# Kernel optimization log

Measured on AMD Instinct MI355X. Metric: run time of the kernel, lower is better.

Reference implementation:

```python
import jax, jax.numpy as jnp
import numpy as np


def _pdists(X):
    # Pairwise Euclidean distances (torch.cdist, p=2) via the Gram trick.
    sq = jnp.sum(X * X, axis=1)                      # (bs,)
    d2 = sq[:, None] + sq[None, :] - 2.0 * (X @ X.T)  # (bs, bs)
    d2 = jnp.maximum(d2, 0.0)
    # safe sqrt: exact forward, finite gradient at 0
    pos = d2 > 0
    return jnp.where(pos, jnp.sqrt(jnp.where(pos, d2, 1.0)), 0.0)


def setup_inputs() -> dict:
    key = jax.random.key(0)
    k1, k2, k3 = jax.random.split(key, 3)
    bs, d = 4096, 512
    n_classes, n_domains = 4, 3
    X = jax.random.normal(k1, (bs, d), dtype=jnp.float32)
    ds = jax.random.randint(k2, (bs,), 0, n_domains, dtype=jnp.int64 if jax.config.read('jax_enable_x64') else jnp.int32)
    y = jax.random.randint(k3, (bs,), 0, n_classes, dtype=jnp.int64 if jax.config.read('jax_enable_x64') else jnp.int32)
    return {"X": X, "ds": ds, "y": y, "n_classes": n_classes, "n_domains": n_domains}


def reference(X, ds, y, n_classes, n_domains):
    # Equivalent to JointCCSA.LSA / JointCCSA.LS with norm=True, assuming every
    # class and domain value appears in the batch (what torch.unique would find).
    dists = _pdists(X)                                # (bs, bs)

    d_lt = ds[:, None] < ds[None, :]                  # domain pair (d1 < d2) ordering
    same_y = y[:, None] == y[None, :]
    y_lt = y[:, None] < y[None, :]                    # class pair (c1 < c2) ordering

    # SA loss: 0.5 * sum over (i,j) with y_i==y_j, ds_i<ds_j
    sa_loss = 0.5 * jnp.sum(jnp.where(same_y & d_lt, dists, 0.0))
    n_sa = n_classes * (n_domains * (n_domains - 1) // 2)
    sa_loss = sa_loss / n_sa

    # S loss: hinge on margin=1, 0.5 * sum over (i,j) with y_i<y_j, ds_i<ds_j
    margin = 1.0
    h = jnp.maximum(0.0, margin - dists)
    s_loss = 0.5 * jnp.sum(jnp.where(y_lt & d_lt, h, 0.0))
    n_s = (n_classes * (n_classes - 1) // 2) * (n_domains * (n_domains - 1) // 2)
    s_loss = s_loss / n_s

    return sa_loss, s_loss
```

## Files before the change

### kernel.cpp

```cpp
#include <hip/hip_runtime.h>
#include <hip/hip_bf16.h>
#include <stdint.h>

#define NROW 4096
#define DIM  512
#define BM   128
#define BN   128
#define BK   32
#define NKT  (DIM / BK)

typedef __attribute__((ext_vector_type(8))) short  short8;
typedef __attribute__((ext_vector_type(4))) float  floatx4;

typedef const __attribute__((address_space(1))) void gvoid_t;
typedef __attribute__((address_space(3))) void       svoid_t;

__device__ __forceinline__ unsigned short f32_to_bf16_rne(float f) {
    unsigned u = __float_as_uint(f);
    u += 0x7FFFu + ((u >> 16) & 1u);
    return (unsigned short)(u >> 16);
}

__global__ __launch_bounds__(256) void prep_kernel(
    const float* __restrict__ X, const int* __restrict__ ds,
    const int* __restrict__ y, unsigned short* __restrict__ Xpre,
    float2* __restrict__ meta, float* __restrict__ out)
{
    const int wave = threadIdx.x >> 6;
    const int lane = threadIdx.x & 63;
    const int row  = blockIdx.x * 4 + wave;
    const float4* xr = (const float4*)(X + (size_t)row * DIM);
    float4 v0 = xr[2 * lane];
    float4 v1 = xr[2 * lane + 1];
    float s = v0.x*v0.x + v0.y*v0.y + v0.z*v0.z + v0.w*v0.w
            + v1.x*v1.x + v1.y*v1.y + v1.z*v1.z + v1.w*v1.w;
    uint4 pk;
    pk.x = f32_to_bf16_rne(v0.x) | ((unsigned)f32_to_bf16_rne(v0.y) << 16);
    pk.y = f32_to_bf16_rne(v0.z) | ((unsigned)f32_to_bf16_rne(v0.w) << 16);
    pk.z = f32_to_bf16_rne(v1.x) | ((unsigned)f32_to_bf16_rne(v1.y) << 16);
    pk.w = f32_to_bf16_rne(v1.z) | ((unsigned)f32_to_bf16_rne(v1.w) << 16);
    const int G     = row >> 3;
    const int l3r   = row & 7;
    const int kt32  = lane >> 2;
    const int chunk = lane & 3;
    const int p     = chunk ^ (row & 3);
    *(uint4*)(Xpre + ((size_t)kt32 * 512 + G) * 256 + l3r * 32 + p * 8) = pk;
    #pragma unroll
    for (int off = 32; off; off >>= 1) s += __shfl_xor(s, off);
    if (lane == 0)
        meta[row] = make_float2(s, __int_as_float(y[row] * 4 + ds[row]));
    if (blockIdx.x == 0 && threadIdx.x < 2) out[threadIdx.x] = 0.0f;
}

__global__ __launch_bounds__(512, 6) void ccsa_kernel(
    const unsigned short* __restrict__ Xpre, const float2* __restrict__ meta,
    const int* __restrict__ ncls, const int* __restrict__ ndom,
    float* __restrict__ out)
{
    __shared__ __align__(16) unsigned short As[2 * BM * BK];
    __shared__ __align__(16) unsigned short Bs[2 * BN * BK];
    __shared__ float red[16];

    const int t = blockIdx.x;
    int r = (int)((sqrtf(8.0f * (float)t + 1.0f) - 1.0f) * 0.5f);
    while ((r + 1) * (r + 2) / 2 <= t) ++r;
    while (r * (r + 1) / 2 > t) --r;
    const int bj_t = r;
    const int bi_t = t - r * (r + 1) / 2;
    const bool diag = (bi_t == bj_t);
    const int bm0 = bi_t * BM;
    const int bn0 = bj_t * BN;
    const int GA = bm0 >> 3;
    const int GB = bn0 >> 3;

    const int tid    = threadIdx.x;
    const int wave   = tid >> 6;
    const int lane   = tid & 63;
    const int warp_m = wave >> 2;
    const int warp_n = wave & 3;
    const int m15    = lane & 15;
    const int quad   = lane >> 4;
    const int sw     = m15 & 3;

    float sqj[2]; int yj[2], dj[2];
    #pragma unroll
    for (int tn = 0; tn < 2; ++tn) {
        const float2 mj = meta[bn0 + warp_n * 32 + tn * 16 + m15];
        sqj[tn] = mj.x;
        const int ydj = __float_as_int(mj.y);
        dj[tn] = ydj & 3; yj[tn] = ydj >> 2;
    }

    floatx4 acc[4][2];
    #pragma unroll
    for (int a = 0; a < 4; ++a)
        #pragma unroll
        for (int b = 0; b < 2; ++b)
            acc[a][b] = (floatx4){0.f, 0.f, 0.f, 0.f};

    const unsigned short* Bbase = diag ? As : Bs;

    #define STAGE(buf, kt)                                                    \
        do {                                                                  \
            __builtin_amdgcn_global_load_lds(                                 \
                (gvoid_t*)(Xpre + ((size_t)(kt) * 512 + GA) * 256 + tid * 8), \
                (svoid_t*)(&As[(buf) * 4096 + tid * 8]), 16, 0, 0);           \
            if (!diag)                                                        \
                __builtin_amdgcn_global_load_lds(                             \
                    (gvoid_t*)(Xpre + ((size_t)(kt) * 512 + GB) * 256         \
                               + tid * 8),                                    \
                    (svoid_t*)(&Bs[(buf) * 4096 + tid * 8]), 16, 0, 0);       \
        } while (0)

    const int physA = (quad ^ sw) * 8;

    STAGE(0, 0);
    for (int kt = 0; kt < NKT; ++kt) {
        const int cur = kt & 1;
        __syncthreads();
        if (kt + 1 < NKT) STAGE(cur ^ 1, kt + 1);

        short8 a[4], b[2];
        #pragma unroll
        for (int tt = 0; tt < 4; ++tt) {
            const int rla = warp_m * 64 + tt * 16 + m15;
            a[tt] = *(const short8*)(&As[cur * 4096 + rla * 32 + physA]);
        }
        #pragma unroll
        for (int tt = 0; tt < 2; ++tt) {
            const int rlb = warp_n * 32 + tt * 16 + m15;
            b[tt] = *(const short8*)(&Bbase[cur * 4096 + rlb * 32 + physA]);
        }
        #pragma unroll
        for (int tm = 0; tm < 4; ++tm)
            #pragma unroll
            for (int tn = 0; tn < 2; ++tn)
                acc[tm][tn] = __builtin_amdgcn_mfma_f32_16x16x32_bf16(
                    a[tm], b[tn], acc[tm][tn], 0, 0, 0);
    }
    #undef STAGE

    float sa = 0.f, ss = 0.f;
    #pragma unroll
    for (int tm = 0; tm < 4; ++tm) {
        #pragma unroll
        for (int rr = 0; rr < 4; ++rr) {
            const int i = bm0 + warp_m * 64 + tm * 16 + quad * 4 + rr;
            const float2 mi = meta[i];
            const int ydi = __float_as_int(mi.y);
            const int di = ydi & 3, yi = ydi >> 2;
            #pragma unroll
            for (int tn = 0; tn < 2; ++tn) {
                if (diag) {
                    if (di < dj[tn]) {
                        const float d2   = mi.x + sqj[tn] - 2.0f * acc[tm][tn][rr];
                        const float dist = sqrtf(fmaxf(d2, 0.f));
                        if (yi == yj[tn])     sa += dist;
                        else if (yi < yj[tn]) ss += fmaxf(0.f, 1.f - dist);
                    }
                } else {
                    if (di != dj[tn]) {
                        const float d2   = mi.x + sqj[tn] - 2.0f * acc[tm][tn][rr];
                        const float dist = sqrtf(fmaxf(d2, 0.f));
                        if (yi == yj[tn]) {
                            sa += dist;
                        } else {
                            const bool take = (di < dj[tn]) ? (yi < yj[tn])
                                                            : (yj[tn] < yi);
                            if (take) ss += fmaxf(0.f, 1.f - dist);
                        }
                    }
                }
            }
        }
    }
    #pragma unroll
    for (int off = 32; off; off >>= 1) {
        sa += __shfl_xor(sa, off);
        ss += __shfl_xor(ss, off);
    }
    if (lane == 0) { red[wave] = sa; red[8 + wave] = ss; }
    __syncthreads();
    if (tid == 0) {
        float tsa = 0.f, tss = 0.f;
        #pragma unroll
        for (int w = 0; w < 8; ++w) { tsa += red[w]; tss += red[8 + w]; }
        const int nc = *ncls, nd = *ndom;
        const float n_sa = (float)(nc * (nd * (nd - 1) / 2));
        const float n_s  = (float)((nc * (nc - 1) / 2) * (nd * (nd - 1) / 2));
        atomicAdd(out + 0, tsa * 0.5f / n_sa);
        atomicAdd(out + 1, tss * 0.5f / n_s);
    }
}

extern "C" void kernel_launch(void* const* d_in, const int* in_sizes, int n_in,
                              void* d_out, int out_size, void* d_ws, size_t ws_size,
                              hipStream_t stream) {
    (void)in_sizes; (void)n_in; (void)out_size; (void)ws_size;
    const float* X  = (const float*)d_in[0];
    const int*   ds = (const int*)d_in[1];
    const int*   y  = (const int*)d_in[2];
    const int*   nc = (const int*)d_in[3];
    const int*   nd = (const int*)d_in[4];
    float* out = (float*)d_out;

    unsigned short* Xpre = (unsigned short*)d_ws;
    float2* meta = (float2*)((char*)d_ws + (size_t)NROW * DIM * 2);

    prep_kernel<<<NROW / 4, 256, 0, stream>>>(X, ds, y, Xpre, meta, out);
    const int ntiles = NROW / BM;
    const int nblocks = ntiles * (ntiles + 1) / 2;
    ccsa_kernel<<<nblocks, 512, 0, stream>>>(Xpre, meta, nc, nd, out);
}
```

Measured before the change: 100.4 us.

## Switch Gram matmul to FP8 MFMA with 64x64 tiles and whole-panel LDS loads

Quantizes X to FP8 in the prep kernel instead of BF16 and uses fp8 16x16x32 MFMAs for the Gram product. Tiles shrink to 64x64 with 256 threads, and each block loads both full 64x512 K panels into LDS at once through an XOR-swizzled layout, replacing the double-buffered K loop. This halves the operand bytes and doubles the number of blocks. The cost is much lower precision in the distances, especially near the hinge margin, and the larger LDS footprint per block limits occupancy.

```diff
diff --git a/kernel.cpp b/kernel.cpp
--- a/kernel.cpp
+++ b/kernel.cpp
@@ -4,26 +4,19 @@
 
 #define NROW 4096
 #define DIM  512
-#define BM   128
-#define BN   128
-#define BK   32
-#define NKT  (DIM / BK)
+#define BT   64
+#define NT64 (NROW / BT)
+#define NTRI (NT64 * (NT64 + 1) / 2)
+#define PANEL (BT * DIM)
 
-typedef __attribute__((ext_vector_type(8))) short  short8;
-typedef __attribute__((ext_vector_type(4))) float  floatx4;
+typedef __attribute__((ext_vector_type(4))) float floatx4;
 
 typedef const __attribute__((address_space(1))) void gvoid_t;
 typedef __attribute__((address_space(3))) void       svoid_t;
 
-__device__ __forceinline__ unsigned short f32_to_bf16_rne(float f) {
-    unsigned u = __float_as_uint(f);
-    u += 0x7FFFu + ((u >> 16) & 1u);
-    return (unsigned short)(u >> 16);
-}
-
 __global__ __launch_bounds__(256) void prep_kernel(
     const float* __restrict__ X, const int* __restrict__ ds,
-    const int* __restrict__ y, unsigned short* __restrict__ Xpre,
+    const int* __restrict__ y, unsigned char* __restrict__ Xq,
     float2* __restrict__ meta, float* __restrict__ out)
 {
     const int wave = threadIdx.x >> 6;
@@ -34,17 +27,15 @@
     float4 v1 = xr[2 * lane + 1];
     float s = v0.x*v0.x + v0.y*v0.y + v0.z*v0.z + v0.w*v0.w
             + v1.x*v1.x + v1.y*v1.y + v1.z*v1.z + v1.w*v1.w;
-    uint4 pk;
-    pk.x = f32_to_bf16_rne(v0.x) | ((unsigned)f32_to_bf16_rne(v0.y) << 16);
-    pk.y = f32_to_bf16_rne(v0.z) | ((unsigned)f32_to_bf16_rne(v0.w) << 16);
-    pk.z = f32_to_bf16_rne(v1.x) | ((unsigned)f32_to_bf16_rne(v1.y) << 16);
-    pk.w = f32_to_bf16_rne(v1.z) | ((unsigned)f32_to_bf16_rne(v1.w) << 16);
-    const int G     = row >> 3;
-    const int l3r   = row & 7;
-    const int kt32  = lane >> 2;
-    const int chunk = lane & 3;
-    const int p     = chunk ^ (row & 3);
-    *(uint4*)(Xpre + ((size_t)kt32 * 512 + G) * 256 + l3r * 32 + p * 8) = pk;
+    int q0 = __builtin_amdgcn_cvt_pk_fp8_f32(v0.x, v0.y, 0, false);
+    q0     = __builtin_amdgcn_cvt_pk_fp8_f32(v0.z, v0.w, q0, true);
+    int q1 = __builtin_amdgcn_cvt_pk_fp8_f32(v1.x, v1.y, 0, false);
+    q1     = __builtin_amdgcn_cvt_pk_fp8_f32(v1.z, v1.w, q1, true);
+    const int g  = row >> 6;
+    const int r6 = row & 63;
+    const int p  = lane ^ r6;
+    *(uint2*)(Xq + (size_t)g * PANEL + r6 * 512 + p * 8) =
+        make_uint2((unsigned)q0, (unsigned)q1);
     #pragma unroll
     for (int off = 32; off; off >>= 1) s += __shfl_xor(s, off);
     if (lane == 0)
@@ -52,100 +43,89 @@
     if (blockIdx.x == 0 && threadIdx.x < 2) out[threadIdx.x] = 0.0f;
 }
 
-__global__ __launch_bounds__(512, 6) void ccsa_kernel(
-    const unsigned short* __restrict__ Xpre, const float2* __restrict__ meta,
+__global__ __launch_bounds__(256, 2) void ccsa_kernel(
+    const unsigned char* __restrict__ Xq, const float2* __restrict__ meta,
     const int* __restrict__ ncls, const int* __restrict__ ndom,
     float* __restrict__ out)
 {
-    __shared__ __align__(16) unsigned short As[2 * BM * BK];
-    __shared__ __align__(16) unsigned short Bs[2 * BN * BK];
-    __shared__ float red[16];
+    __shared__ __align__(16) unsigned char As[PANEL];
+    __shared__ __align__(16) unsigned char Bs[PANEL];
+    __shared__ float red[8];
 
     const int t = blockIdx.x;
     int r = (int)((sqrtf(8.0f * (float)t + 1.0f) - 1.0f) * 0.5f);
     while ((r + 1) * (r + 2) / 2 <= t) ++r;
     while (r * (r + 1) / 2 > t) --r;
-    const int bj_t = r;
-    const int bi_t = t - r * (r + 1) / 2;
-    const bool diag = (bi_t == bj_t);
-    const int bm0 = bi_t * BM;
-    const int bn0 = bj_t * BN;
-    const int GA = bm0 >> 3;
-    const int GB = bn0 >> 3;
+    const int jt   = r;
+    const int it   = t - r * (r + 1) / 2;
+    const bool diag = (it == jt);
+    const int i0 = it * BT;
+    const int j0 = jt * BT;
 
     const int tid    = threadIdx.x;
     const int wave   = tid >> 6;
     const int lane   = tid & 63;
-    const int warp_m = wave >> 2;
-    const int warp_n = wave & 3;
+    const int warp_m = wave >> 1;
+    const int warp_n = wave & 1;
     const int m15    = lane & 15;
     const int quad   = lane >> 4;
-    const int sw     = m15 & 3;
 
     float sqj[2]; int yj[2], dj[2];
     #pragma unroll
     for (int tn = 0; tn < 2; ++tn) {
-        const float2 mj = meta[bn0 + warp_n * 32 + tn * 16 + m15];
+        const float2 mj = meta[j0 + warp_n * 32 + tn * 16 + m15];
         sqj[tn] = mj.x;
         const int ydj = __float_as_int(mj.y);
         dj[tn] = ydj & 3; yj[tn] = ydj >> 2;
     }
 
-    floatx4 acc[4][2];
+    floatx4 acc[2][2];
     #pragma unroll
-    for (int a = 0; a < 4; ++a)
+    for (int a = 0; a < 2; ++a)
         #pragma unroll
         for (int b = 0; b < 2; ++b)
             acc[a][b] = (floatx4){0.f, 0.f, 0.f, 0.f};
 
-    const unsigned short* Bbase = diag ? As : Bs;
+    const unsigned char* srcA = Xq + (size_t)it * PANEL;
+    const unsigned char* srcB = Xq + (size_t)jt * PANEL;
+    #pragma unroll
+    for (int s = 0; s < 8; ++s) {
+        __builtin_amdgcn_global_load_lds(
+            (gvoid_t*)(srcA + s * 4096 + tid * 16),
+            (svoid_t*)(&As[s * 4096 + tid * 16]), 16, 0, 0);
+        if (!diag)
+            __builtin_amdgcn_global_load_lds(
+                (gvoid_t*)(srcB + s * 4096 + tid * 16),
+                (svoid_t*)(&Bs[s * 4096 + tid * 16]), 16, 0, 0);
+    }
+    __syncthreads();
 
-    #define STAGE(buf, kt)                                                    \
-        do {                                                                  \
-            __builtin_amdgcn_global_load_lds(                                 \
-                (gvoid_t*)(Xpre + ((size_t)(kt) * 512 + GA) * 256 + tid * 8), \
-                (svoid_t*)(&As[(buf) * 4096 + tid * 8]), 16, 0, 0);           \
-            if (!diag)                                                        \
-                __builtin_amdgcn_global_load_lds(                             \
-                    (gvoid_t*)(Xpre + ((size_t)(kt) * 512 + GB) * 256         \
-                               + tid * 8),                                    \
-                    (svoid_t*)(&Bs[(buf) * 4096 + tid * 8]), 16, 0, 0);       \
-        } while (0)
+    const unsigned char* Bb = diag ? As : Bs;
 
-    const int physA = (quad ^ sw) * 8;
+    const int rowa0 = warp_m * 32 + m15;
+    const int rowa1 = warp_m * 32 + 16 + m15;
+    const int rowb0 = warp_n * 32 + m15;
+    const int rowb1 = warp_n * 32 + 16 + m15;
 
-    STAGE(0, 0);
-    for (int kt = 0; kt < NKT; ++kt) {
-        const int cur = kt & 1;
-        __syncthreads();
-        if (kt + 1 < NKT) STAGE(cur ^ 1, kt + 1);
-
-        short8 a[4], b[2];
-        #pragma unroll
-        for (int tt = 0; tt < 4; ++tt) {
-            const int rla = warp_m * 64 + tt * 16 + m15;
-            a[tt] = *(const short8*)(&As[cur * 4096 + rla * 32 + physA]);
-        }
-        #pragma unroll
-        for (int tt = 0; tt < 2; ++tt) {
-            const int rlb = warp_n * 32 + tt * 16 + m15;
-            b[tt] = *(const short8*)(&Bbase[cur * 4096 + rlb * 32 + physA]);
-        }
-        #pragma unroll
-        for (int tm = 0; tm < 4; ++tm)
-            #pragma unroll
-            for (int tn = 0; tn < 2; ++tn)
-                acc[tm][tn] = __builtin_amdgcn_mfma_f32_16x16x32_bf16(
-                    a[tm], b[tn], acc[tm][tn], 0, 0, 0);
+    #pragma unroll
+    for (int kt = 0; kt < 16; ++kt) {
+        const int c = kt * 4 + quad;
+        const long a0 = *(const long*)(&As[rowa0 * 512 + (c ^ rowa0) * 8]);
+        const long a1 = *(const long*)(&As[rowa1 * 512 + (c ^ rowa1) * 8]);
+        const long b0 = *(const long*)(&Bb[rowb0 * 512 + (c ^ rowb0) * 8]);
+        const long b1 = *(const long*)(&Bb[rowb1 * 512 + (c ^ rowb1) * 8]);
+        acc[0][0] = __builtin_amdgcn_mfma_f32_16x16x32_fp8_fp8(a0, b0, acc[0][0], 0, 0, 0);
+        acc[0][1] = __builtin_amdgcn_mfma_f32_16x16x32_fp8_fp8(a0, b1, acc[0][1], 0, 0, 0);
+        acc[1][0] = __builtin_amdgcn_mfma_f32_16x16x32_fp8_fp8(a1, b0, acc[1][0], 0, 0, 0);
+        acc[1][1] = __builtin_amdgcn_mfma_f32_16x16x32_fp8_fp8(a1, b1, acc[1][1], 0, 0, 0);
     }
-    #undef STAGE
 
     float sa = 0.f, ss = 0.f;
     #pragma unroll
-    for (int tm = 0; tm < 4; ++tm) {
+    for (int tm = 0; tm < 2; ++tm) {
         #pragma unroll
         for (int rr = 0; rr < 4; ++rr) {
-            const int i = bm0 + warp_m * 64 + tm * 16 + quad * 4 + rr;
+            const int i = i0 + warp_m * 32 + tm * 16 + quad * 4 + rr;
             const float2 mi = meta[i];
             const int ydi = __float_as_int(mi.y);
             const int di = ydi & 3, yi = ydi >> 2;
@@ -179,12 +159,11 @@
         sa += __shfl_xor(sa, off);
         ss += __shfl_xor(ss, off);
     }
-    if (lane == 0) { red[wave] = sa; red[8 + wave] = ss; }
+    if (lane == 0) { red[wave] = sa; red[4 + wave] = ss; }
     __syncthreads();
     if (tid == 0) {
-        float tsa = 0.f, tss = 0.f;
-        #pragma unroll
-        for (int w = 0; w < 8; ++w) { tsa += red[w]; tss += red[8 + w]; }
+        const float tsa = red[0] + red[1] + red[2] + red[3];
+        const float tss = red[4] + red[5] + red[6] + red[7];
         const int nc = *ncls, nd = *ndom;
         const float n_sa = (float)(nc * (nd * (nd - 1) / 2));
         const float n_s  = (float)((nc * (nc - 1) / 2) * (nd * (nd - 1) / 2));
@@ -204,11 +183,9 @@
     const int*   nd = (const int*)d_in[4];
     float* out = (float*)d_out;
 
-    unsigned short* Xpre = (unsigned short*)d_ws;
-    float2* meta = (float2*)((char*)d_ws + (size_t)NROW * DIM * 2);
+    unsigned char* Xq = (unsigned char*)d_ws;
+    float2* meta = (float2*)((char*)d_ws + (size_t)NT64 * PANEL);
 
-    prep_kernel<<<NROW / 4, 256, 0, stream>>>(X, ds, y, Xpre, meta, out);
-    const int ntiles = NROW / BM;
-    const int nblocks = ntiles * (ntiles + 1) / 2;
-    ccsa_kernel<<<nblocks, 512, 0, stream>>>(Xpre, meta, nc, nd, out);
+    prep_kernel<<<NROW / 4, 256, 0, stream>>>(X, ds, y, Xq, meta, out);
+    ccsa_kernel<<<NTRI, 256, 0, stream>>>(Xq, meta, nc, nd, out);
 }
```

New measurement: 126.5 us. +26.0%, slower.

## Quantize Gram matrix inputs to FP8 and use FP8 MFMA with larger K tiles

Applied to the files above, without the earlier changes.

The prep kernel now packs X as FP8 instead of BF16, in a new swizzled layout of 128-byte K panels. The distance kernel switches to fp8 MFMA with a K tile of 128 bytes per row, so there are 4 k-iterations instead of 16 and fewer barriers. This halves the bytes loaded from global memory and LDS. The risk is accuracy: norms stay in fp32, but the dot products lose precision, which may hurt distances near the margin. LDS use grows and the launch bound for occupancy drops from 6 to 4.

```diff
diff --git a/kernel.cpp b/kernel.cpp
--- a/kernel.cpp
+++ b/kernel.cpp
@@ -6,24 +6,18 @@
 #define DIM  512
 #define BM   128
 #define BN   128
-#define BK   32
-#define NKT  (DIM / BK)
-
-typedef __attribute__((ext_vector_type(8))) short  short8;
-typedef __attribute__((ext_vector_type(4))) float  floatx4;
+#define BKE  128
+#define NKT  (DIM / BKE)
+#define PANEL_KT (BM * BKE)
+
+typedef __attribute__((ext_vector_type(4))) float floatx4;
 
 typedef const __attribute__((address_space(1))) void gvoid_t;
 typedef __attribute__((address_space(3))) void       svoid_t;
 
-__device__ __forceinline__ unsigned short f32_to_bf16_rne(float f) {
-    unsigned u = __float_as_uint(f);
-    u += 0x7FFFu + ((u >> 16) & 1u);
-    return (unsigned short)(u >> 16);
-}
-
 __global__ __launch_bounds__(256) void prep_kernel(
     const float* __restrict__ X, const int* __restrict__ ds,
-    const int* __restrict__ y, unsigned short* __restrict__ Xpre,
+    const int* __restrict__ y, unsigned char* __restrict__ Xq,
     float2* __restrict__ meta, float* __restrict__ out)
 {
     const int wave = threadIdx.x >> 6;
@@ -34,17 +28,17 @@
     float4 v1 = xr[2 * lane + 1];
     float s = v0.x*v0.x + v0.y*v0.y + v0.z*v0.z + v0.w*v0.w
             + v1.x*v1.x + v1.y*v1.y + v1.z*v1.z + v1.w*v1.w;
-    uint4 pk;
-    pk.x = f32_to_bf16_rne(v0.x) | ((unsigned)f32_to_bf16_rne(v0.y) << 16);
-    pk.y = f32_to_bf16_rne(v0.z) | ((unsigned)f32_to_bf16_rne(v0.w) << 16);
-    pk.z = f32_to_bf16_rne(v1.x) | ((unsigned)f32_to_bf16_rne(v1.y) << 16);
-    pk.w = f32_to_bf16_rne(v1.z) | ((unsigned)f32_to_bf16_rne(v1.w) << 16);
-    const int G     = row >> 3;
-    const int l3r   = row & 7;
-    const int kt32  = lane >> 2;
-    const int chunk = lane & 3;
-    const int p     = chunk ^ (row & 3);
-    *(uint4*)(Xpre + ((size_t)kt32 * 512 + G) * 256 + l3r * 32 + p * 8) = pk;
+    int q0 = __builtin_amdgcn_cvt_pk_fp8_f32(v0.x, v0.y, 0, false);
+    q0     = __builtin_amdgcn_cvt_pk_fp8_f32(v0.z, v0.w, q0, true);
+    int q1 = __builtin_amdgcn_cvt_pk_fp8_f32(v1.x, v1.y, 0, false);
+    q1     = __builtin_amdgcn_cvt_pk_fp8_f32(v1.z, v1.w, q1, true);
+    const int g8  = row >> 3;
+    const int l3r = row & 7;
+    const int kt  = lane >> 4;
+    const int c   = lane & 15;
+    const int p8  = c ^ (row & 15);
+    *(uint2*)(Xq + ((size_t)(kt * 512 + g8) * 8 + l3r) * 128 + p8 * 8) =
+        make_uint2((unsigned)q0, (unsigned)q1);
     #pragma unroll
     for (int off = 32; off; off >>= 1) s += __shfl_xor(s, off);
     if (lane == 0)
@@ -52,13 +46,13 @@
     if (blockIdx.x == 0 && threadIdx.x < 2) out[threadIdx.x] = 0.0f;
 }
 
-__global__ __launch_bounds__(512, 6) void ccsa_kernel(
-    const unsigned short* __restrict__ Xpre, const float2* __restrict__ meta,
+__global__ __launch_bounds__(512, 4) void ccsa_kernel(
+    const unsigned char* __restrict__ Xq, const float2* __restrict__ meta,
     const int* __restrict__ ncls, const int* __restrict__ ndom,
     float* __restrict__ out)
 {
-    __shared__ __align__(16) unsigned short As[2 * BM * BK];
-    __shared__ __align__(16) unsigned short Bs[2 * BN * BK];
+    __shared__ __align__(16) unsigned char As[2 * PANEL_KT];
+    __shared__ __align__(16) unsigned char Bs[2 * PANEL_KT];
     __shared__ float red[16];
 
     const int t = blockIdx.x;
@@ -80,7 +74,6 @@
     const int warp_n = wave & 3;
     const int m15    = lane & 15;
     const int quad   = lane >> 4;
-    const int sw     = m15 & 3;
 
     float sqj[2]; int yj[2], dj[2];
     #pragma unroll
@@ -98,45 +91,64 @@
         for (int b = 0; b < 2; ++b)
             acc[a][b] = (floatx4){0.f, 0.f, 0.f, 0.f};
 
-    const unsigned short* Bbase = diag ? As : Bs;
+    const unsigned char* Bb = diag ? As : Bs;
 
     #define STAGE(buf, kt)                                                    \
         do {                                                                  \
+            const unsigned char* srcA =                                       \
+                Xq + (size_t)((kt) * 512 + GA) * 1024;                        \
             __builtin_amdgcn_global_load_lds(                                 \
-                (gvoid_t*)(Xpre + ((size_t)(kt) * 512 + GA) * 256 + tid * 8), \
-                (svoid_t*)(&As[(buf) * 4096 + tid * 8]), 16, 0, 0);           \
-            if (!diag)                                                        \
+                (gvoid_t*)(srcA + tid * 16),                                  \
+                (svoid_t*)(&As[(buf) * PANEL_KT + tid * 16]), 16, 0, 0);      \
+            __builtin_amdgcn_global_load_lds(                                 \
+                (gvoid_t*)(srcA + 8192 + tid * 16),                           \
+                (svoid_t*)(&As[(buf) * PANEL_KT + 8192 + tid * 16]),          \
+                16, 0, 0);                                                    \
+            if (!diag) {                                                      \
+                const unsigned char* srcB =                                   \
+                    Xq + (size_t)((kt) * 512 + GB) * 1024;                    \
                 __builtin_amdgcn_global_load_lds(                             \
-                    (gvoid_t*)(Xpre + ((size_t)(kt) * 512 + GB) * 256         \
-                               + tid * 8),                                    \
-                    (svoid_t*)(&Bs[(buf) * 4096 + tid * 8]), 16, 0, 0);       \
+                    (gvoid_t*)(srcB + tid * 16),                              \
+                    (svoid_t*)(&Bs[(buf) * PANEL_KT + tid * 16]), 16, 0, 0);  \
+                __builtin_amdgcn_global_load_lds(                             \
+                    (gvoid_t*)(srcB + 8192 + tid * 16),                       \
+                    (svoid_t*)(&Bs[(buf) * PANEL_KT + 8192 + tid * 16]),      \
+                    16, 0, 0);                                                \
+            }                                                                 \
         } while (0)
 
-    const int physA = (quad ^ sw) * 8;
+    const int rla0 = (warp_m * 64 +  0 + m15) * 128;
+    const int rla1 = (warp_m * 64 + 16 + m15) * 128;
+    const int rla2 = (warp_m * 64 + 32 + m15) * 128;
+    const int rla3 = (warp_m * 64 + 48 + m15) * 128;
+    const int rlb0 = (warp_n * 32 +  0 + m15) * 128;
+    const int rlb1 = (warp_n * 32 + 16 + m15) * 128;
 
     STAGE(0, 0);
     for (int kt = 0; kt < NKT; ++kt) {
         const int cur = kt & 1;
         __syncthreads();
         if (kt + 1 < NKT) STAGE(cur ^ 1, kt + 1);
-
-        short8 a[4], b[2];
-        #pragma unroll
-        for (int tt = 0; tt < 4; ++tt) {
-            const int rla = warp_m * 64 + tt * 16 + m15;
-            a[tt] = *(const short8*)(&As[cur * 4096 + rla * 32 + physA]);
+        const int cb = cur * PANEL_KT;
+
+        #pragma unroll
+        for (int s = 0; s < 4; ++s) {
+            const int ph = ((s * 4 + quad) ^ m15) * 8;
+            const long a0 = *(const long*)(&As[cb + rla0 + ph]);
+            const long a1 = *(const long*)(&As[cb + rla1 + ph]);
+            const long a2 = *(const long*)(&As[cb + rla2 + ph]);
+            const long a3 = *(const long*)(&As[cb + rla3 + ph]);
+            const long b0 = *(const long*)(&Bb[cb + rlb0 + ph]);
+            const long b1 = *(const long*)(&Bb[cb + rlb1 + ph]);
+            acc[0][0] = __builtin_amdgcn_mfma_f32_16x16x32_fp8_fp8(a0, b0, acc[0][0], 0, 0, 0);
+            acc[0][1] = __builtin_amdgcn_mfma_f32_16x16x32_fp8_fp8(a0, b1, acc[0][1], 0, 0, 0);
+            acc[1][0] = __builtin_amdgcn_mfma_f32_16x16x32_fp8_fp8(a1, b0, acc[1][0], 0, 0, 0);
+            acc[1][1] = __builtin_amdgcn_mfma_f32_16x16x32_fp8_fp8(a1, b1, acc[1][1], 0, 0, 0);
+            acc[2][0] = __builtin_amdgcn_mfma_f32_16x16x32_fp8_fp8(a2, b0, acc[2][0], 0, 0, 0);
+            acc[2][1] = __builtin_amdgcn_mfma_f32_16x16x32_fp8_fp8(a2, b1, acc[2][1], 0, 0, 0);
+            acc[3][0] = __builtin_amdgcn_mfma_f32_16x16x32_fp8_fp8(a3, b0, acc[3][0], 0, 0, 0);
+            acc[3][1] = __builtin_amdgcn_mfma_f32_16x16x32_fp8_fp8(a3, b1, acc[3][1], 0, 0, 0);
         }
-        #pragma unroll
-        for (int tt = 0; tt < 2; ++tt) {
-            const int rlb = warp_n * 32 + tt * 16 + m15;
-            b[tt] = *(const short8*)(&Bbase[cur * 4096 + rlb * 32 + physA]);
-        }
-        #pragma unroll
-        for (int tm = 0; tm < 4; ++tm)
-            #pragma unroll
-            for (int tn = 0; tn < 2; ++tn)
-                acc[tm][tn] = __builtin_amdgcn_mfma_f32_16x16x32_bf16(
-                    a[tm], b[tn], acc[tm][tn], 0, 0, 0);
     }
     #undef STAGE
 
@@ -204,11 +216,11 @@
     const int*   nd = (const int*)d_in[4];
     float* out = (float*)d_out;
 
-    unsigned short* Xpre = (unsigned short*)d_ws;
-    float2* meta = (float2*)((char*)d_ws + (size_t)NROW * DIM * 2);
-
-    prep_kernel<<<NROW / 4, 256, 0, stream>>>(X, ds, y, Xpre, meta, out);
+    unsigned char* Xq = (unsigned char*)d_ws;
+    float2* meta = (float2*)((char*)d_ws + (size_t)NROW * DIM);
+
+    prep_kernel<<<NROW / 4, 256, 0, stream>>>(X, ds, y, Xq, meta, out);
     const int ntiles = NROW / BM;
     const int nblocks = ntiles * (ntiles + 1) / 2;
-    ccsa_kernel<<<nblocks, 512, 0, stream>>>(Xpre, meta, nc, nd, out);
+    ccsa_kernel<<<nblocks, 512, 0, stream>>>(Xq, meta, nc, nd, out);
 }
```

New measurement: 97.34 us. 3.1% less time.
